# Kernel optimization log

Measured on AMD Instinct MI355X. Metric: run time of the kernel, lower is better.

## Reference

```python
import jax, jax.numpy as jnp
import numpy as np

B, S, D = 1, 4096, 512
QK_DIM, N_HEADS = 512, 8
HEAD_DIM = QK_DIM // N_HEADS


def setup_inputs() -> dict:
    key = jax.random.key(0)
    ks = jax.random.split(key, 9)
    s_in = 1.0 / np.sqrt(D)
    s_v = 1.0 / np.sqrt(QK_DIM)
    return {
        "x": jax.random.normal(ks[0], (B, S, D), dtype=jnp.float32),
        # torch nn.Linear convention: weight (out_features, in_features)
        "Wq": jax.random.uniform(ks[1], (QK_DIM, D), jnp.float32, -s_in, s_in),
        "bq": jax.random.uniform(ks[2], (QK_DIM,), jnp.float32, -s_in, s_in),
        "Wk": jax.random.uniform(ks[3], (QK_DIM, D), jnp.float32, -s_in, s_in),
        "bk": jax.random.uniform(ks[4], (QK_DIM,), jnp.float32, -s_in, s_in),
        "Wv": jax.random.uniform(ks[5], (QK_DIM, D), jnp.float32, -s_in, s_in),
        "bv": jax.random.uniform(ks[6], (QK_DIM,), jnp.float32, -s_in, s_in),
        "Wo": jax.random.uniform(ks[7], (D, QK_DIM), jnp.float32, -s_v, s_v),
        "bo": jax.random.uniform(ks[8], (D,), jnp.float32, -s_v, s_v),
    }


def reference(x, Wq, bq, Wk, bk, Wv, bv, Wo, bo):
    # Faithful to source: tokens flattened over batch*seq before head split.
    n = x.shape[0] * x.shape[1]  # B*S
    Q = (x @ Wq.T + bq).reshape(n, N_HEADS, HEAD_DIM).transpose(1, 0, 2)  # (H, N, hd)
    K = (x @ Wk.T + bk).reshape(n, N_HEADS, HEAD_DIM).transpose(1, 0, 2)
    V = (x @ Wv.T + bv).reshape(n, N_HEADS, HEAD_DIM).transpose(1, 0, 2)
    scores = jnp.einsum("hnd,hmd->hnm", Q, K) / np.sqrt(HEAD_DIM).astype(np.float32)
    attn = jax.nn.softmax(scores, axis=-1)                # (H, N, N) materialized
    ctx = jnp.einsum("hnm,hmd->hnd", attn, V)             # (H, N, hd)
    ctx = ctx.transpose(1, 0, 2).reshape(n, QK_DIM)       # (N, qk_dim)
    return ctx @ Wo.T + bo                                # (N, input_dim)
```

## Files before the change

### kernel.cpp

```cpp
#include <hip/hip_runtime.h>
#include <math.h>

#define N_TOK 4096
#define DMODEL 512
#define NH 8
#define HD 64

typedef __attribute__((ext_vector_type(4))) float f32x4;
typedef __attribute__((ext_vector_type(8))) _Float16 f16x8;
typedef __attribute__((ext_vector_type(4))) _Float16 f16x4;

#define MFMA16(A, B, C) __builtin_amdgcn_mfma_f32_16x16x32_f16(A, B, C, 0, 0, 0)

__global__ __launch_bounds__(256) void qkv_gemm(const float* __restrict__ x,
                                                const float* __restrict__ Wq,
                                                const float* __restrict__ bq,
                                                const float* __restrict__ Wk,
                                                const float* __restrict__ bk,
                                                const float* __restrict__ Wv,
                                                const float* __restrict__ bv,
                                                _Float16* __restrict__ Q16,
                                                _Float16* __restrict__ K16,
                                                _Float16* __restrict__ VT16) {
    __shared__ __align__(16) _Float16 As[64][72];
    __shared__ __align__(16) _Float16 Ws[64][72];
    int z = blockIdx.z;
    const float* W = (z == 0) ? Wq : (z == 1) ? Wk : Wv;
    const float* bias = (z == 0) ? bq : (z == 1) ? bk : bv;

    int n0 = blockIdx.x * 64, o0 = blockIdx.y * 64;
    int t = threadIdx.x;
    int w = t >> 6, l = t & 63, quad = l >> 4, ln = l & 15;
    int srow = t >> 2, scol = (t & 3) * 16;

    f32x4 acc[4] = {};

    for (int k0 = 0; k0 < DMODEL; k0 += 64) {
        __syncthreads();
        {
            const float* Ap = x + (size_t)(n0 + srow) * DMODEL + k0 + scol;
            f32x4 a0 = *(const f32x4*)Ap;
            f32x4 a1 = *(const f32x4*)(Ap + 4);
            f32x4 a2 = *(const f32x4*)(Ap + 8);
            f32x4 a3 = *(const f32x4*)(Ap + 12);
            const float* Wp = W + (size_t)(o0 + srow) * DMODEL + k0 + scol;
            f32x4 w0 = *(const f32x4*)Wp;
            f32x4 w1 = *(const f32x4*)(Wp + 4);
            f32x4 w2 = *(const f32x4*)(Wp + 8);
            f32x4 w3 = *(const f32x4*)(Wp + 12);
            f16x8 aa = {(_Float16)a0[0], (_Float16)a0[1], (_Float16)a0[2], (_Float16)a0[3],
                        (_Float16)a1[0], (_Float16)a1[1], (_Float16)a1[2], (_Float16)a1[3]};
            f16x8 ab = {(_Float16)a2[0], (_Float16)a2[1], (_Float16)a2[2], (_Float16)a2[3],
                        (_Float16)a3[0], (_Float16)a3[1], (_Float16)a3[2], (_Float16)a3[3]};
            f16x8 wa = {(_Float16)w0[0], (_Float16)w0[1], (_Float16)w0[2], (_Float16)w0[3],
                        (_Float16)w1[0], (_Float16)w1[1], (_Float16)w1[2], (_Float16)w1[3]};
            f16x8 wb = {(_Float16)w2[0], (_Float16)w2[1], (_Float16)w2[2], (_Float16)w2[3],
                        (_Float16)w3[0], (_Float16)w3[1], (_Float16)w3[2], (_Float16)w3[3]};
            *(f16x8*)&As[srow][scol] = aa;
            *(f16x8*)&As[srow][scol + 8] = ab;
            *(f16x8*)&Ws[srow][scol] = wa;
            *(f16x8*)&Ws[srow][scol + 8] = wb;
        }
        __syncthreads();
#pragma unroll
        for (int ks = 0; ks < 2; ks++) {
            f16x8 af = *(const f16x8*)&As[w * 16 + ln][ks * 32 + quad * 8];
#pragma unroll
            for (int c = 0; c < 4; c++) {
                f16x8 bf = *(const f16x8*)&Ws[c * 16 + ln][ks * 32 + quad * 8];
                acc[c] = MFMA16(af, bf, acc[c]);
            }
        }
    }

    int h = o0 >> 6;
#pragma unroll
    for (int c = 0; c < 4; c++) {
        float bv_ = bias[o0 + c * 16 + ln];
#pragma unroll
        for (int i = 0; i < 4; i++) {
            int r = n0 + w * 16 + quad * 4 + i;
            float v = acc[c][i] + bv_;
            if (z == 0) {
                Q16[((size_t)h * N_TOK + r) * HD + c * 16 + ln] = (_Float16)(v * 0.125f);
            } else if (z == 1) {
                K16[((size_t)h * N_TOK + r) * HD + c * 16 + ln] = (_Float16)v;
            } else {
                int kp = quad * 16 + i * 4 + w;
                VT16[((size_t)h * HD + c * 16 + ln) * N_TOK + n0 + kp] = (_Float16)v;
            }
        }
    }
}

__global__ __launch_bounds__(256) void out_gemm(const _Float16* __restrict__ A,
                                                const float* __restrict__ W,
                                                const float* __restrict__ bias,
                                                float* __restrict__ dst) {
    __shared__ __align__(16) _Float16 As[64][72];
    __shared__ __align__(16) _Float16 Ws[64][72];
    int n0 = blockIdx.x * 64, o0 = blockIdx.y * 64;
    int t = threadIdx.x;
    int w = t >> 6, l = t & 63, quad = l >> 4, ln = l & 15;
    int srow = t >> 2, scol = (t & 3) * 16;

    f32x4 acc[4] = {};

    for (int k0 = 0; k0 < DMODEL; k0 += 64) {
        __syncthreads();
        {
            const _Float16* Ap = A + (size_t)(n0 + srow) * DMODEL + k0 + scol;
            f16x8 a0 = *(const f16x8*)Ap;
            f16x8 a1 = *(const f16x8*)(Ap + 8);
            const float* Wp = W + (size_t)(o0 + srow) * DMODEL + k0 + scol;
            f32x4 w0 = *(const f32x4*)Wp;
            f32x4 w1 = *(const f32x4*)(Wp + 4);
            f32x4 w2 = *(const f32x4*)(Wp + 8);
            f32x4 w3 = *(const f32x4*)(Wp + 12);
            *(f16x8*)&As[srow][scol] = a0;
            *(f16x8*)&As[srow][scol + 8] = a1;
            f16x8 wa = {(_Float16)w0[0], (_Float16)w0[1], (_Float16)w0[2], (_Float16)w0[3],
                        (_Float16)w1[0], (_Float16)w1[1], (_Float16)w1[2], (_Float16)w1[3]};
            f16x8 wb = {(_Float16)w2[0], (_Float16)w2[1], (_Float16)w2[2], (_Float16)w2[3],
                        (_Float16)w3[0], (_Float16)w3[1], (_Float16)w3[2], (_Float16)w3[3]};
            *(f16x8*)&Ws[srow][scol] = wa;
            *(f16x8*)&Ws[srow][scol + 8] = wb;
        }
        __syncthreads();
#pragma unroll
        for (int ks = 0; ks < 2; ks++) {
            f16x8 af = *(const f16x8*)&As[w * 16 + ln][ks * 32 + quad * 8];
#pragma unroll
            for (int c = 0; c < 4; c++) {
                f16x8 bf = *(const f16x8*)&Ws[c * 16 + ln][ks * 32 + quad * 8];
                acc[c] = MFMA16(af, bf, acc[c]);
            }
        }
    }

#pragma unroll
    for (int c = 0; c < 4; c++) {
        float bv_ = bias[o0 + c * 16 + ln];
#pragma unroll
        for (int i = 0; i < 4; i++) {
            int r = n0 + w * 16 + quad * 4 + i;
            dst[(size_t)r * DMODEL + o0 + c * 16 + ln] = acc[c][i] + bv_;
        }
    }
}

__global__ __launch_bounds__(256) void flash_mfma(const _Float16* __restrict__ Q16,
                                                  const _Float16* __restrict__ K16,
                                                  const _Float16* __restrict__ VT16,
                                                  _Float16* __restrict__ ctx) {
    __shared__ __align__(16) _Float16 Ks[64][72];
    __shared__ __align__(16) _Float16 Vs[64][72];
    __shared__ __align__(16) _Float16 Ps[4][32][72];

    int t = threadIdx.x;
    int w = t >> 6, l = t & 63, quad = l >> 4, ln = l & 15;
    int bid = blockIdx.x;
    int h = bid & 7;
    int n0 = (bid >> 3) * 128;

    f16x8 qf[2][2];
#pragma unroll
    for (int rt = 0; rt < 2; rt++) {
        const _Float16* qp =
            &Q16[((size_t)h * N_TOK + n0 + w * 32 + rt * 16 + ln) * HD + quad * 8];
        qf[rt][0] = *(const f16x8*)qp;
        qf[rt][1] = *(const f16x8*)(qp + 32);
    }

    f32x4 oacc[2][4] = {};
    f32x4 lsum[2] = {};

    const _Float16* kbase = K16 + (size_t)h * N_TOK * HD;
    const _Float16* vbase = VT16 + (size_t)h * HD * N_TOK;
    int srow = t >> 2, scol = (t & 3) * 16;

    f16x8 pk0, pk1, pv0, pv1;
    {
        const _Float16* kp = kbase + t * 16;
        pk0 = *(const f16x8*)kp;
        pk1 = *(const f16x8*)(kp + 8);
        const _Float16* vp = vbase + (size_t)srow * N_TOK + scol;
        pv0 = *(const f16x8*)vp;
        pv1 = *(const f16x8*)(vp + 8);
    }

    for (int m0 = 0; m0 < N_TOK; m0 += 64) {
        __syncthreads();
        *(f16x8*)&Ks[srow][scol] = pk0;
        *(f16x8*)&Ks[srow][scol + 8] = pk1;
        *(f16x8*)&Vs[srow][scol] = pv0;
        *(f16x8*)&Vs[srow][scol + 8] = pv1;
        __syncthreads();

        int m1 = m0 + 64;
        if (m1 < N_TOK) {
            const _Float16* kp = kbase + (size_t)m1 * HD + t * 16;
            pk0 = *(const f16x8*)kp;
            pk1 = *(const f16x8*)(kp + 8);
            const _Float16* vp = vbase + (size_t)srow * N_TOK + m1 + scol;
            pv0 = *(const f16x8*)vp;
            pv1 = *(const f16x8*)(vp + 8);
        }

        f16x8 kb[4][2];
#pragma unroll
        for (int c = 0; c < 4; c++) {
            kb[c][0] = *(const f16x8*)&Ks[c * 16 + ln][quad * 8];
            kb[c][1] = *(const f16x8*)&Ks[c * 16 + ln][32 + quad * 8];
        }
#pragma unroll
        for (int rt = 0; rt < 2; rt++) {
            f32x4 sacc[4] = {};
#pragma unroll
            for (int c = 0; c < 4; c++) {
                sacc[c] = MFMA16(qf[rt][0], kb[c][0], sacc[c]);
                sacc[c] = MFMA16(qf[rt][1], kb[c][1], sacc[c]);
            }
#pragma unroll
            for (int i = 0; i < 4; i++) {
                float p0 = __expf(sacc[0][i]);
                float p1 = __expf(sacc[1][i]);
                float p2 = __expf(sacc[2][i]);
                float p3 = __expf(sacc[3][i]);
                lsum[rt][i] += (p0 + p1) + (p2 + p3);
                f16x4 pv = {(_Float16)p0, (_Float16)p1, (_Float16)p2, (_Float16)p3};
                *(f16x4*)&Ps[w][rt * 16 + quad * 4 + i][ln * 4] = pv;
            }
        }

        f16x8 vb[4][2];
#pragma unroll
        for (int c = 0; c < 4; c++) {
            vb[c][0] = *(const f16x8*)&Vs[c * 16 + ln][quad * 8];
            vb[c][1] = *(const f16x8*)&Vs[c * 16 + ln][32 + quad * 8];
        }
#pragma unroll
        for (int rt = 0; rt < 2; rt++) {
            f16x8 a0 = *(const f16x8*)&Ps[w][rt * 16 + ln][quad * 8];
            f16x8 a1 = *(const f16x8*)&Ps[w][rt * 16 + ln][32 + quad * 8];
#pragma unroll
            for (int c = 0; c < 4; c++) {
                oacc[rt][c] = MFMA16(a0, vb[c][0], oacc[rt][c]);
                oacc[rt][c] = MFMA16(a1, vb[c][1], oacc[rt][c]);
            }
        }
    }

#pragma unroll
    for (int d = 1; d < 16; d <<= 1)
#pragma unroll
        for (int rt = 0; rt < 2; rt++)
#pragma unroll
            for (int i = 0; i < 4; i++) lsum[rt][i] += __shfl_xor(lsum[rt][i], d, 64);

#pragma unroll
    for (int rt = 0; rt < 2; rt++)
#pragma unroll
        for (int c = 0; c < 4; c++)
#pragma unroll
            for (int i = 0; i < 4; i++) {
                int r = n0 + w * 32 + rt * 16 + quad * 4 + i;
                ctx[(size_t)r * DMODEL + h * HD + c * 16 + ln] =
                    (_Float16)(oacc[rt][c][i] / lsum[rt][i]);
            }
}

extern "C" void kernel_launch(void* const* d_in, const int* in_sizes, int n_in,
                              void* d_out, int out_size, void* d_ws, size_t ws_size,
                              hipStream_t stream) {
    const float* x  = (const float*)d_in[0];
    const float* Wq = (const float*)d_in[1];
    const float* bq = (const float*)d_in[2];
    const float* Wk = (const float*)d_in[3];
    const float* bk = (const float*)d_in[4];
    const float* Wv = (const float*)d_in[5];
    const float* bv = (const float*)d_in[6];
    const float* Wo = (const float*)d_in[7];
    const float* bo = (const float*)d_in[8];
    float* out = (float*)d_out;

    float* ws = (float*)d_ws;
    _Float16* Q16   = (_Float16*)(ws);
    _Float16* K16   = (_Float16*)(ws + (1u << 20));
    _Float16* VT16  = (_Float16*)(ws + (2u << 20));
    _Float16* CTX16 = (_Float16*)(ws + (3u << 20));

    qkv_gemm<<<dim3(64, 8, 3), 256, 0, stream>>>(x, Wq, bq, Wk, bk, Wv, bv,
                                                 Q16, K16, VT16);
    flash_mfma<<<dim3(256), 256, 0, stream>>>(Q16, K16, VT16, CTX16);
    out_gemm<<<dim3(64, 8), 256, 0, stream>>>(CTX16, Wo, bo, out);
}
```

Baseline: 178.6 us.

## Split attention over key range, pre-cast inputs to fp16, retile QKV GEMM

Adds a cast kernel that converts x and all weights to fp16 once. The QKV GEMM gets larger 128-row tiles with register prefetch of the next k-tile. The flash kernel moves to 512-thread blocks that read K and V directly from global memory and use a swizzled P buffer. It also applies exp2 with log2e folded into the Q scale, and splits the key range into four partitions, writing partial outputs and row sums. The output GEMM reduces the four partials and normalizes them while loading, which costs extra memory traffic and an additional launch.

```diff
diff --git a/kernel.cpp b/kernel.cpp
--- a/kernel.cpp
+++ b/kernel.cpp
@@ -12,119 +12,266 @@
 
 #define MFMA16(A, B, C) __builtin_amdgcn_mfma_f32_16x16x32_f16(A, B, C, 0, 0, 0)
 
-__global__ __launch_bounds__(256) void qkv_gemm(const float* __restrict__ x,
+__global__ __launch_bounds__(256) void cast_all(const float* __restrict__ x,
                                                 const float* __restrict__ Wq,
+                                                const float* __restrict__ Wk,
+                                                const float* __restrict__ Wv,
+                                                const float* __restrict__ Wo,
+                                                _Float16* __restrict__ X16,
+                                                _Float16* __restrict__ W16) {
+    const int NX = N_TOK * DMODEL;
+    const int NW = DMODEL * DMODEL;
+    int i = (blockIdx.x * 256 + threadIdx.x) * 8;
+    const float* src;
+    _Float16* dst;
+    int off;
+    if (i < NX) {
+        src = x; dst = X16; off = i;
+    } else {
+        int j = i - NX;
+        int seg = j >> 18;
+        off = j & (NW - 1);
+        src = (seg == 0) ? Wq : (seg == 1) ? Wk : (seg == 2) ? Wv : Wo;
+        dst = W16 + (size_t)seg * NW;
+    }
+    f32x4 a = *(const f32x4*)&src[off];
+    f32x4 b = *(const f32x4*)&src[off + 4];
+    f16x8 o = {(_Float16)a[0], (_Float16)a[1], (_Float16)a[2], (_Float16)a[3],
+               (_Float16)b[0], (_Float16)b[1], (_Float16)b[2], (_Float16)b[3]};
+    *(f16x8*)&dst[off] = o;
+}
+
+__global__ __launch_bounds__(256) void qkv_gemm(const _Float16* __restrict__ X16,
+                                                const _Float16* __restrict__ W16,
                                                 const float* __restrict__ bq,
-                                                const float* __restrict__ Wk,
                                                 const float* __restrict__ bk,
-                                                const float* __restrict__ Wv,
                                                 const float* __restrict__ bv,
                                                 _Float16* __restrict__ Q16,
                                                 _Float16* __restrict__ K16,
                                                 _Float16* __restrict__ VT16) {
-    __shared__ __align__(16) _Float16 As[64][72];
+    __shared__ __align__(16) _Float16 As[128][72];
     __shared__ __align__(16) _Float16 Ws[64][72];
     int z = blockIdx.z;
-    const float* W = (z == 0) ? Wq : (z == 1) ? Wk : Wv;
+    const _Float16* W = W16 + (size_t)z * DMODEL * DMODEL;
     const float* bias = (z == 0) ? bq : (z == 1) ? bk : bv;
 
-    int n0 = blockIdx.x * 64, o0 = blockIdx.y * 64;
+    int n0 = blockIdx.x * 128, o0 = blockIdx.y * 64;
     int t = threadIdx.x;
     int w = t >> 6, l = t & 63, quad = l >> 4, ln = l & 15;
-    int srow = t >> 2, scol = (t & 3) * 16;
-
-    f32x4 acc[4] = {};
+    int sr = t >> 3, sc = (t & 7) * 8;
+
+    const _Float16* Abase = X16 + (size_t)n0 * DMODEL;
+    const _Float16* Wbase = W + (size_t)o0 * DMODEL;
+
+    f32x4 acc[2][4] = {};
+
+    f16x8 pa[4], pw[2];
+#pragma unroll
+    for (int r = 0; r < 4; r++) pa[r] = *(const f16x8*)&Abase[(size_t)(sr + r * 32) * DMODEL + sc];
+#pragma unroll
+    for (int r = 0; r < 2; r++) pw[r] = *(const f16x8*)&Wbase[(size_t)(sr + r * 32) * DMODEL + sc];
 
     for (int k0 = 0; k0 < DMODEL; k0 += 64) {
         __syncthreads();
-        {
-            const float* Ap = x + (size_t)(n0 + srow) * DMODEL + k0 + scol;
-            f32x4 a0 = *(const f32x4*)Ap;
-            f32x4 a1 = *(const f32x4*)(Ap + 4);
-            f32x4 a2 = *(const f32x4*)(Ap + 8);
-            f32x4 a3 = *(const f32x4*)(Ap + 12);
-            const float* Wp = W + (size_t)(o0 + srow) * DMODEL + k0 + scol;
-            f32x4 w0 = *(const f32x4*)Wp;
-            f32x4 w1 = *(const f32x4*)(Wp + 4);
-            f32x4 w2 = *(const f32x4*)(Wp + 8);
-            f32x4 w3 = *(const f32x4*)(Wp + 12);
-            f16x8 aa = {(_Float16)a0[0], (_Float16)a0[1], (_Float16)a0[2], (_Float16)a0[3],
-                        (_Float16)a1[0], (_Float16)a1[1], (_Float16)a1[2], (_Float16)a1[3]};
-            f16x8 ab = {(_Float16)a2[0], (_Float16)a2[1], (_Float16)a2[2], (_Float16)a2[3],
-                        (_Float16)a3[0], (_Float16)a3[1], (_Float16)a3[2], (_Float16)a3[3]};
-            f16x8 wa = {(_Float16)w0[0], (_Float16)w0[1], (_Float16)w0[2], (_Float16)w0[3],
-                        (_Float16)w1[0], (_Float16)w1[1], (_Float16)w1[2], (_Float16)w1[3]};
-            f16x8 wb = {(_Float16)w2[0], (_Float16)w2[1], (_Float16)w2[2], (_Float16)w2[3],
-                        (_Float16)w3[0], (_Float16)w3[1], (_Float16)w3[2], (_Float16)w3[3]};
-            *(f16x8*)&As[srow][scol] = aa;
-            *(f16x8*)&As[srow][scol + 8] = ab;
-            *(f16x8*)&Ws[srow][scol] = wa;
-            *(f16x8*)&Ws[srow][scol + 8] = wb;
-        }
+#pragma unroll
+        for (int r = 0; r < 4; r++) *(f16x8*)&As[sr + r * 32][sc] = pa[r];
+#pragma unroll
+        for (int r = 0; r < 2; r++) *(f16x8*)&Ws[sr + r * 32][sc] = pw[r];
         __syncthreads();
+
+        int k1 = k0 + 64;
+        if (k1 < DMODEL) {
+#pragma unroll
+            for (int r = 0; r < 4; r++)
+                pa[r] = *(const f16x8*)&Abase[(size_t)(sr + r * 32) * DMODEL + k1 + sc];
+#pragma unroll
+            for (int r = 0; r < 2; r++)
+                pw[r] = *(const f16x8*)&Wbase[(size_t)(sr + r * 32) * DMODEL + k1 + sc];
+        }
+
 #pragma unroll
         for (int ks = 0; ks < 2; ks++) {
-            f16x8 af = *(const f16x8*)&As[w * 16 + ln][ks * 32 + quad * 8];
+            f16x8 af0 = *(const f16x8*)&As[w * 32 + ln][ks * 32 + quad * 8];
+            f16x8 af1 = *(const f16x8*)&As[w * 32 + 16 + ln][ks * 32 + quad * 8];
 #pragma unroll
             for (int c = 0; c < 4; c++) {
                 f16x8 bf = *(const f16x8*)&Ws[c * 16 + ln][ks * 32 + quad * 8];
-                acc[c] = MFMA16(af, bf, acc[c]);
+                acc[0][c] = MFMA16(af0, bf, acc[0][c]);
+                acc[1][c] = MFMA16(af1, bf, acc[1][c]);
             }
         }
     }
 
     int h = o0 >> 6;
+    const float QS = 0.125f * 1.44269504088896340736f;
 #pragma unroll
     for (int c = 0; c < 4; c++) {
         float bv_ = bias[o0 + c * 16 + ln];
 #pragma unroll
-        for (int i = 0; i < 4; i++) {
-            int r = n0 + w * 16 + quad * 4 + i;
-            float v = acc[c][i] + bv_;
-            if (z == 0) {
-                Q16[((size_t)h * N_TOK + r) * HD + c * 16 + ln] = (_Float16)(v * 0.125f);
-            } else if (z == 1) {
-                K16[((size_t)h * N_TOK + r) * HD + c * 16 + ln] = (_Float16)v;
-            } else {
-                int kp = quad * 16 + i * 4 + w;
-                VT16[((size_t)h * HD + c * 16 + ln) * N_TOK + n0 + kp] = (_Float16)v;
-            }
-        }
-    }
-}
-
-__global__ __launch_bounds__(256) void out_gemm(const _Float16* __restrict__ A,
-                                                const float* __restrict__ W,
-                                                const float* __restrict__ bias,
-                                                float* __restrict__ dst) {
+        for (int rt = 0; rt < 2; rt++) {
+#pragma unroll
+            for (int i = 0; i < 4; i++) {
+                int lr = w * 32 + rt * 16 + quad * 4 + i;
+                int n = n0 + lr;
+                float v = acc[rt][c][i] + bv_;
+                if (z == 0) {
+                    Q16[((size_t)h * N_TOK + n) * HD + c * 16 + ln] = (_Float16)(v * QS);
+                } else if (z == 1) {
+                    K16[((size_t)h * N_TOK + n) * HD + c * 16 + ln] = (_Float16)v;
+                } else {
+                    int kp = (quad * 4 + i) * 4 + (w & 1) * 2 + rt;
+                    VT16[((size_t)h * HD + c * 16 + ln) * N_TOK + n0 + (w >> 1) * 64 + kp] =
+                        (_Float16)v;
+                }
+            }
+        }
+    }
+}
+
+__global__ __launch_bounds__(512, 2) void flash_mfma(const _Float16* __restrict__ Q16,
+                                                     const _Float16* __restrict__ K16,
+                                                     const _Float16* __restrict__ VT16,
+                                                     _Float16* __restrict__ OP,
+                                                     float* __restrict__ LS) {
+    __shared__ __align__(16) _Float16 Ps[8][64][64];
+
+    int t = threadIdx.x;
+    int w = t >> 6, l = t & 63, quad = l >> 4, ln = l & 15;
+    int bid = blockIdx.x;
+    int h = bid & 7;
+    int qt = (bid >> 3) & 7;
+    int s = bid >> 6;
+    int q0 = qt * 512 + w * 64;
+    int m_start = s * 1024;
+
+    const _Float16* qbase = Q16 + ((size_t)h * N_TOK + q0) * HD;
+    f16x8 qf[4][2];
+#pragma unroll
+    for (int rt = 0; rt < 4; rt++) {
+        const _Float16* qp = qbase + (size_t)(rt * 16 + ln) * HD + quad * 8;
+        qf[rt][0] = *(const f16x8*)qp;
+        qf[rt][1] = *(const f16x8*)(qp + 32);
+    }
+
+    f32x4 oacc[4][4] = {};
+    f32x4 lsum[4] = {};
+
+    const _Float16* kbase = K16 + (size_t)h * N_TOK * HD;
+    const _Float16* vbase = VT16 + (size_t)h * HD * N_TOK;
+    int swz = (ln & 7) * 8;
+
+    for (int m0 = m_start; m0 < m_start + 1024; m0 += 64) {
+        f16x8 kb[4][2];
+#pragma unroll
+        for (int c = 0; c < 4; c++) {
+            const _Float16* kp = kbase + (size_t)(m0 + c * 16 + ln) * HD + quad * 8;
+            kb[c][0] = *(const f16x8*)kp;
+            kb[c][1] = *(const f16x8*)(kp + 32);
+        }
+#pragma unroll
+        for (int rt = 0; rt < 4; rt++) {
+            f32x4 sacc[4] = {};
+#pragma unroll
+            for (int c = 0; c < 4; c++) {
+                sacc[c] = MFMA16(qf[rt][0], kb[c][0], sacc[c]);
+                sacc[c] = MFMA16(qf[rt][1], kb[c][1], sacc[c]);
+            }
+#pragma unroll
+            for (int i = 0; i < 4; i++) {
+                float p0 = __builtin_exp2f(sacc[0][i]);
+                float p1 = __builtin_exp2f(sacc[1][i]);
+                float p2 = __builtin_exp2f(sacc[2][i]);
+                float p3 = __builtin_exp2f(sacc[3][i]);
+                lsum[rt][i] += (p0 + p1) + (p2 + p3);
+                f16x4 pv = {(_Float16)p0, (_Float16)p1, (_Float16)p2, (_Float16)p3};
+                int row = quad * 4 + i;
+                *(f16x4*)&Ps[w][rt * 16 + row][(ln * 4) ^ ((row & 7) * 8)] = pv;
+            }
+        }
+        f16x8 vb[4][2];
+#pragma unroll
+        for (int c = 0; c < 4; c++) {
+            const _Float16* vp = vbase + (size_t)(c * 16 + ln) * N_TOK + m0 + quad * 8;
+            vb[c][0] = *(const f16x8*)vp;
+            vb[c][1] = *(const f16x8*)(vp + 32);
+        }
+#pragma unroll
+        for (int rt = 0; rt < 4; rt++) {
+            f16x8 a0 = *(const f16x8*)&Ps[w][rt * 16 + ln][(quad * 8) ^ swz];
+            f16x8 a1 = *(const f16x8*)&Ps[w][rt * 16 + ln][(32 + quad * 8) ^ swz];
+#pragma unroll
+            for (int c = 0; c < 4; c++) {
+                oacc[rt][c] = MFMA16(a0, vb[c][0], oacc[rt][c]);
+                oacc[rt][c] = MFMA16(a1, vb[c][1], oacc[rt][c]);
+            }
+        }
+    }
+
+#pragma unroll
+    for (int d = 1; d < 16; d <<= 1)
+#pragma unroll
+        for (int rt = 0; rt < 4; rt++)
+#pragma unroll
+            for (int i = 0; i < 4; i++) lsum[rt][i] += __shfl_xor(lsum[rt][i], d, 64);
+
+    _Float16* obase = OP + (size_t)s * N_TOK * DMODEL;
+#pragma unroll
+    for (int rt = 0; rt < 4; rt++)
+#pragma unroll
+        for (int c = 0; c < 4; c++)
+#pragma unroll
+            for (int i = 0; i < 4; i++) {
+                int r = q0 + rt * 16 + quad * 4 + i;
+                obase[(size_t)r * DMODEL + h * HD + c * 16 + ln] = (_Float16)oacc[rt][c][i];
+            }
+    if (ln == 0) {
+#pragma unroll
+        for (int rt = 0; rt < 4; rt++)
+#pragma unroll
+            for (int i = 0; i < 4; i++) {
+                int r = q0 + rt * 16 + quad * 4 + i;
+                LS[((size_t)s * NH + h) * N_TOK + r] = lsum[rt][i];
+            }
+    }
+}
+
+__global__ __launch_bounds__(256) void out_gemm(const _Float16* __restrict__ OP,
+                                                const float* __restrict__ LS,
+                                                const _Float16* __restrict__ Wo16,
+                                                const float* __restrict__ bo,
+                                                float* __restrict__ out) {
     __shared__ __align__(16) _Float16 As[64][72];
     __shared__ __align__(16) _Float16 Ws[64][72];
     int n0 = blockIdx.x * 64, o0 = blockIdx.y * 64;
     int t = threadIdx.x;
     int w = t >> 6, l = t & 63, quad = l >> 4, ln = l & 15;
-    int srow = t >> 2, scol = (t & 3) * 16;
+    int sr = t >> 3, sc = (t & 7) * 8;
+    const size_t PSTR = (size_t)N_TOK * DMODEL;
 
     f32x4 acc[4] = {};
 
     for (int k0 = 0; k0 < DMODEL; k0 += 64) {
+        int h = k0 >> 6;
         __syncthreads();
-        {
-            const _Float16* Ap = A + (size_t)(n0 + srow) * DMODEL + k0 + scol;
-            f16x8 a0 = *(const f16x8*)Ap;
-            f16x8 a1 = *(const f16x8*)(Ap + 8);
-            const float* Wp = W + (size_t)(o0 + srow) * DMODEL + k0 + scol;
-            f32x4 w0 = *(const f32x4*)Wp;
-            f32x4 w1 = *(const f32x4*)(Wp + 4);
-            f32x4 w2 = *(const f32x4*)(Wp + 8);
-            f32x4 w3 = *(const f32x4*)(Wp + 12);
-            *(f16x8*)&As[srow][scol] = a0;
-            *(f16x8*)&As[srow][scol + 8] = a1;
-            f16x8 wa = {(_Float16)w0[0], (_Float16)w0[1], (_Float16)w0[2], (_Float16)w0[3],
-                        (_Float16)w1[0], (_Float16)w1[1], (_Float16)w1[2], (_Float16)w1[3]};
-            f16x8 wb = {(_Float16)w2[0], (_Float16)w2[1], (_Float16)w2[2], (_Float16)w2[3],
-                        (_Float16)w3[0], (_Float16)w3[1], (_Float16)w3[2], (_Float16)w3[3]};
-            *(f16x8*)&Ws[srow][scol] = wa;
-            *(f16x8*)&Ws[srow][scol + 8] = wb;
+#pragma unroll
+        for (int r = 0; r < 2; r++) {
+            int row = sr + r * 32;
+            int n = n0 + row;
+            size_t base = (size_t)n * DMODEL + k0 + sc;
+            f16x8 a0 = *(const f16x8*)&OP[base];
+            f16x8 a1 = *(const f16x8*)&OP[PSTR + base];
+            f16x8 a2 = *(const f16x8*)&OP[2 * PSTR + base];
+            f16x8 a3 = *(const f16x8*)&OP[3 * PSTR + base];
+            const float* ls = LS + (size_t)h * N_TOK + n;
+            float lt = ls[0] + ls[NH * N_TOK] + ls[2 * NH * N_TOK] + ls[3 * NH * N_TOK];
+            float inv = 1.0f / lt;
+            f16x8 o;
+#pragma unroll
+            for (int j = 0; j < 8; j++)
+                o[j] = (_Float16)((((float)a0[j] + (float)a1[j]) +
+                                   ((float)a2[j] + (float)a3[j])) * inv);
+            *(f16x8*)&As[row][sc] = o;
+            *(f16x8*)&Ws[row][sc] = *(const f16x8*)&Wo16[(size_t)(o0 + row) * DMODEL + k0 + sc];
         }
         __syncthreads();
 #pragma unroll
@@ -140,134 +287,13 @@
 
 #pragma unroll
     for (int c = 0; c < 4; c++) {
-        float bv_ = bias[o0 + c * 16 + ln];
+        float bv_ = bo[o0 + c * 16 + ln];
 #pragma unroll
         for (int i = 0; i < 4; i++) {
             int r = n0 + w * 16 + quad * 4 + i;
-            dst[(size_t)r * DMODEL + o0 + c * 16 + ln] = acc[c][i] + bv_;
-        }
-    }
-}
-
-__global__ __launch_bounds__(256) void flash_mfma(const _Float16* __restrict__ Q16,
-                                                  const _Float16* __restrict__ K16,
-                                                  const _Float16* __restrict__ VT16,
-                                                  _Float16* __restrict__ ctx) {
-    __shared__ __align__(16) _Float16 Ks[64][72];
-    __shared__ __align__(16) _Float16 Vs[64][72];
-    __shared__ __align__(16) _Float16 Ps[4][32][72];
-
-    int t = threadIdx.x;
-    int w = t >> 6, l = t & 63, quad = l >> 4, ln = l & 15;
-    int bid = blockIdx.x;
-    int h = bid & 7;
-    int n0 = (bid >> 3) * 128;
-
-    f16x8 qf[2][2];
-#pragma unroll
-    for (int rt = 0; rt < 2; rt++) {
-        const _Float16* qp =
-            &Q16[((size_t)h * N_TOK + n0 + w * 32 + rt * 16 + ln) * HD + quad * 8];
-        qf[rt][0] = *(const f16x8*)qp;
-        qf[rt][1] = *(const f16x8*)(qp + 32);
-    }
-
-    f32x4 oacc[2][4] = {};
-    f32x4 lsum[2] = {};
-
-    const _Float16* kbase = K16 + (size_t)h * N_TOK * HD;
-    const _Float16* vbase = VT16 + (size_t)h * HD * N_TOK;
-    int srow = t >> 2, scol = (t & 3) * 16;
-
-    f16x8 pk0, pk1, pv0, pv1;
-    {
-        const _Float16* kp = kbase + t * 16;
-        pk0 = *(const f16x8*)kp;
-        pk1 = *(const f16x8*)(kp + 8);
-        const _Float16* vp = vbase + (size_t)srow * N_TOK + scol;
-        pv0 = *(const f16x8*)vp;
-        pv1 = *(const f16x8*)(vp + 8);
-    }
-
-    for (int m0 = 0; m0 < N_TOK; m0 += 64) {
-        __syncthreads();
-        *(f16x8*)&Ks[srow][scol] = pk0;
-        *(f16x8*)&Ks[srow][scol + 8] = pk1;
-        *(f16x8*)&Vs[srow][scol] = pv0;
-        *(f16x8*)&Vs[srow][scol + 8] = pv1;
-        __syncthreads();
-
-        int m1 = m0 + 64;
-        if (m1 < N_TOK) {
-            const _Float16* kp = kbase + (size_t)m1 * HD + t * 16;
-            pk0 = *(const f16x8*)kp;
-            pk1 = *(const f16x8*)(kp + 8);
-            const _Float16* vp = vbase + (size_t)srow * N_TOK + m1 + scol;
-            pv0 = *(const f16x8*)vp;
-            pv1 = *(const f16x8*)(vp + 8);
-        }
-
-        f16x8 kb[4][2];
-#pragma unroll
-        for (int c = 0; c < 4; c++) {
-            kb[c][0] = *(const f16x8*)&Ks[c * 16 + ln][quad * 8];
-            kb[c][1] = *(const f16x8*)&Ks[c * 16 + ln][32 + quad * 8];
-        }
-#pragma unroll
-        for (int rt = 0; rt < 2; rt++) {
-            f32x4 sacc[4] = {};
-#pragma unroll
-            for (int c = 0; c < 4; c++) {
-                sacc[c] = MFMA16(qf[rt][0], kb[c][0], sacc[c]);
-                sacc[c] = MFMA16(qf[rt][1], kb[c][1], sacc[c]);
-            }
-#pragma unroll
-            for (int i = 0; i < 4; i++) {
-                float p0 = __expf(sacc[0][i]);
-                float p1 = __expf(sacc[1][i]);
-                float p2 = __expf(sacc[2][i]);
-                float p3 = __expf(sacc[3][i]);
-                lsum[rt][i] += (p0 + p1) + (p2 + p3);
-                f16x4 pv = {(_Float16)p0, (_Float16)p1, (_Float16)p2, (_Float16)p3};
-                *(f16x4*)&Ps[w][rt * 16 + quad * 4 + i][ln * 4] = pv;
-            }
-        }
-
-        f16x8 vb[4][2];
-#pragma unroll
-        for (int c = 0; c < 4; c++) {
-            vb[c][0] = *(const f16x8*)&Vs[c * 16 + ln][quad * 8];
-            vb[c][1] = *(const f16x8*)&Vs[c * 16 + ln][32 + quad * 8];
-        }
-#pragma unroll
-        for (int rt = 0; rt < 2; rt++) {
-            f16x8 a0 = *(const f16x8*)&Ps[w][rt * 16 + ln][quad * 8];
-            f16x8 a1 = *(const f16x8*)&Ps[w][rt * 16 + ln][32 + quad * 8];
-#pragma unroll
-            for (int c = 0; c < 4; c++) {
-                oacc[rt][c] = MFMA16(a0, vb[c][0], oacc[rt][c]);
-                oacc[rt][c] = MFMA16(a1, vb[c][1], oacc[rt][c]);
-            }
-        }
-    }
-
-#pragma unroll
-    for (int d = 1; d < 16; d <<= 1)
-#pragma unroll
-        for (int rt = 0; rt < 2; rt++)
-#pragma unroll
-            for (int i = 0; i < 4; i++) lsum[rt][i] += __shfl_xor(lsum[rt][i], d, 64);
-
-#pragma unroll
-    for (int rt = 0; rt < 2; rt++)
-#pragma unroll
-        for (int c = 0; c < 4; c++)
-#pragma unroll
-            for (int i = 0; i < 4; i++) {
-                int r = n0 + w * 32 + rt * 16 + quad * 4 + i;
-                ctx[(size_t)r * DMODEL + h * HD + c * 16 + ln] =
-                    (_Float16)(oacc[rt][c][i] / lsum[rt][i]);
-            }
+            out[(size_t)r * DMODEL + o0 + c * 16 + ln] = acc[c][i] + bv_;
+        }
+    }
 }
 
 extern "C" void kernel_launch(void* const* d_in, const int* in_sizes, int n_in,
@@ -284,14 +310,20 @@
     const float* bo = (const float*)d_in[8];
     float* out = (float*)d_out;
 
-    float* ws = (float*)d_ws;
-    _Float16* Q16   = (_Float16*)(ws);
-    _Float16* K16   = (_Float16*)(ws + (1u << 20));
-    _Float16* VT16  = (_Float16*)(ws + (2u << 20));
-    _Float16* CTX16 = (_Float16*)(ws + (3u << 20));
-
-    qkv_gemm<<<dim3(64, 8, 3), 256, 0, stream>>>(x, Wq, bq, Wk, bk, Wv, bv,
-                                                 Q16, K16, VT16);
-    flash_mfma<<<dim3(256), 256, 0, stream>>>(Q16, K16, VT16, CTX16);
-    out_gemm<<<dim3(64, 8), 256, 0, stream>>>(CTX16, Wo, bo, out);
-}
+    char* ws = (char*)d_ws;
+    _Float16* X16  = (_Float16*)(ws);
+    _Float16* W16  = (_Float16*)(ws + (4u << 20));
+    _Float16* Q16  = (_Float16*)(ws + (6u << 20));
+    _Float16* K16  = (_Float16*)(ws + (10u << 20));
+    _Float16* VT16 = (_Float16*)(ws + (14u << 20));
+    _Float16* OP   = (_Float16*)(ws + (18u << 20));
+    float*    LSp  = (float*)   (ws + (34u << 20));
+
+    cast_all<<<1536, 256, 0, stream>>>(x, Wq, Wk, Wv, Wo, X16, W16);
+
+    qkv_gemm<<<dim3(32, 8, 3), 256, 0, stream>>>(X16, W16, bq, bk, bv, Q16, K16, VT16);
+
+    flash_mfma<<<dim3(256), 512, 0, stream>>>(Q16, K16, VT16, OP, LSp);
+
+    out_gemm<<<dim3(64, 8), 256, 0, stream>>>(OP, LSp, W16 + 3u * DMODEL * DMODEL, bo, out);
+}
```

Measured after the change: 186.2 us. 4.3% more time.
